# Kernel optimization log

Measured on AMD Instinct MI355X. Metric: run time of the kernel, lower is better.

## Reference

```python
import jax, jax.numpy as jnp
import numpy as np

B, T, D = 4, 8192, 1024
H = 16
HD = D // H  # 64
TOP_K = 64


def setup_inputs() -> dict:
    key = jax.random.key(0)
    ks = jax.random.split(key, 6)
    x = jax.random.normal(ks[0], (B, T, D), dtype=jnp.float32)
    # torch nn.Linear weights are [out, in]; y = x @ W.T
    Wq = jax.random.normal(ks[1], (D, D), dtype=jnp.float32) * 0.02
    Wk = jax.random.normal(ks[2], (D, D), dtype=jnp.float32) * 0.02
    Wv = jax.random.normal(ks[3], (D, D), dtype=jnp.float32) * 0.02
    Wo = jax.random.normal(ks[4], (D, D), dtype=jnp.float32) * 0.02
    # indexer: nn.Linear(head_dim, 1, bias=False) -> weight [1, HD]; keep as [HD]
    w_score = jax.random.normal(ks[5], (HD,), dtype=jnp.float32) * 0.02
    return {"x": x, "Wq": Wq, "Wk": Wk, "Wv": Wv, "Wo": Wo, "w_score": w_score}


def reference(x, Wq, Wk, Wv, Wo, w_score):
    b, t, d = x.shape
    top_k = min(TOP_K, t)
    # projections: [B,T,D] -> [B,H,T,HD]
    def proj(W):
        return jnp.einsum('btd,ed->bte', x, W).reshape(b, t, H, HD).transpose(0, 2, 1, 3)
    q = proj(Wq)
    k = proj(Wk)
    v = proj(Wv)
    # lightning indexer scores: [B,H,T]
    idx_scores = jnp.einsum('bhtd,d->bht', k, w_score)
    _, top_idx = jax.lax.top_k(idx_scores, top_k)  # [B,H,K]
    idx = top_idx[..., None]  # [B,H,K,1]
    k_sparse = jnp.take_along_axis(k, idx, axis=2)  # [B,H,K,HD]
    v_sparse = jnp.take_along_axis(v, idx, axis=2)
    scale = HD ** -0.5
    scores = jnp.einsum('bhtd,bhkd->bhtk', q, k_sparse) * scale  # [B,H,T,K]
    attn = jax.nn.softmax(scores, axis=-1)
    out = jnp.einsum('bhtk,bhkd->bhtd', attn, v_sparse)  # [B,H,T,HD]
    out = out.transpose(0, 2, 1, 3).reshape(b, t, d)
    return jnp.einsum('btd,ed->bte', out, Wo)
```

## Files before the change

kernel.cpp:

```cpp
#include <hip/hip_runtime.h>
#include <hip/hip_bf16.h>
#include <stdint.h>

#define NB 4
#define NT 8192
#define ND 1024
#define NH 16
#define NHD 64
#define NK 64
#define NM (NB*NT)

typedef __attribute__((ext_vector_type(4))) float f32x4;
typedef __attribute__((ext_vector_type(8))) short s16x8;
typedef const void __attribute__((address_space(1)))* gas1_t;
typedef void __attribute__((address_space(3)))* las3_t;

__device__ __forceinline__ float bf2f(ushort u) {
  union { uint32_t i; float f; } v; v.i = ((uint32_t)u) << 16; return v.f;
}
__device__ __forceinline__ ushort f2bf(float f) {
  union { float f; uint32_t i; } v; v.f = f;
  uint32_t r = v.i + 0x7FFFu + ((v.i >> 16) & 1u);
  return (ushort)(r >> 16);
}
__device__ __forceinline__ uint32_t f2ord(uint32_t u) {
  return (u & 0x80000000u) ? ~u : (u | 0x80000000u);
}

__global__ __launch_bounds__(256) void convert_w_kernel(
    const float* __restrict__ Wq, const float* __restrict__ Wk,
    const float* __restrict__ Wv, const float* __restrict__ Wo,
    ushort* __restrict__ wqb, ushort* __restrict__ wkb,
    ushort* __restrict__ wvb, ushort* __restrict__ wob) {
  int i = blockIdx.x * 256 + threadIdx.x;
  wqb[i] = f2bf(Wq[i]); wkb[i] = f2bf(Wk[i]);
  wvb[i] = f2bf(Wv[i]); wob[i] = f2bf(Wo[i]);
}

__global__ __launch_bounds__(256) void prep_u_kernel(
    const float* __restrict__ Wk, const float* __restrict__ wscore,
    ushort* __restrict__ uhi, ushort* __restrict__ ulo) {
  int e = (blockIdx.x & 3) * 256 + threadIdx.x;
  int h = blockIdx.x >> 2;
  float acc = 0.f;
  #pragma unroll 8
  for (int d = 0; d < NHD; ++d) acc += wscore[d] * Wk[(size_t)(h*NHD + d)*ND + e];
  ushort hv = f2bf(acc);
  uhi[h*ND + e] = hv;
  ulo[h*ND + e] = f2bf(acc - bf2f(hv));
}

__global__ __launch_bounds__(256) void prep_x_kernel(
    const float* __restrict__ x, const ushort* __restrict__ uhi,
    const ushort* __restrict__ ulo, ushort* __restrict__ xb,
    float* __restrict__ scores) {
  __shared__ float red[4][2][16][17];
  int t = threadIdx.x, w = t >> 6, l = t & 63;
  int tok0 = blockIdx.x * 32;
  int rs = l & 15, ks8 = (l >> 4) * 8;
  f32x4 acc[2];
  acc[0] = (f32x4){0.f,0.f,0.f,0.f};
  acc[1] = (f32x4){0.f,0.f,0.f,0.f};
  #pragma unroll 2
  for (int ks = 0; ks < 8; ++ks) {
    int kb = w * 256 + ks * 32;
    s16x8 bh = *(const s16x8*)(uhi + rs * ND + kb + ks8);
    s16x8 bl = *(const s16x8*)(ulo + rs * ND + kb + ks8);
    #pragma unroll
    for (int mi = 0; mi < 2; ++mi) {
      const float* xr = x + (size_t)(tok0 + mi*16 + rs) * ND + kb + ks8;
      f32x4 x0 = *(const f32x4*)xr;
      f32x4 x1 = *(const f32x4*)(xr + 4);
      s16x8 hi, lo;
      #pragma unroll
      for (int j = 0; j < 4; ++j) {
        ushort h0 = f2bf(x0[j]);
        hi[j] = (short)h0; lo[j] = (short)f2bf(x0[j] - bf2f(h0));
        ushort h1 = f2bf(x1[j]);
        hi[4+j] = (short)h1; lo[4+j] = (short)f2bf(x1[j] - bf2f(h1));
      }
      *(s16x8*)(xb + (size_t)(tok0 + mi*16 + rs) * ND + kb + ks8) = hi;
      acc[mi] = __builtin_amdgcn_mfma_f32_16x16x32_bf16(hi, bh, acc[mi], 0, 0, 0);
      acc[mi] = __builtin_amdgcn_mfma_f32_16x16x32_bf16(lo, bh, acc[mi], 0, 0, 0);
      acc[mi] = __builtin_amdgcn_mfma_f32_16x16x32_bf16(hi, bl, acc[mi], 0, 0, 0);
    }
  }
  #pragma unroll
  for (int mi = 0; mi < 2; ++mi)
    #pragma unroll
    for (int r = 0; r < 4; ++r)
      red[w][mi][(l >> 4) * 4 + r][l & 15] = acc[mi][r];
  __syncthreads();
  int boff = ((tok0 >> 13) << 4);
  int tt0 = tok0 & (NT - 1);
  #pragma unroll
  for (int it = 0; it < 2; ++it) {
    int tok = t & 31, h = (t >> 5) + it * 8;
    int mi = tok >> 4, row = tok & 15;
    float s = red[0][mi][row][h] + red[1][mi][row][h]
            + red[2][mi][row][h] + red[3][mi][row][h];
    scores[(size_t)(boff + h) * NT + tt0 + tok] = s;
  }
}

__global__ __launch_bounds__(256) void topk_kernel(
    const float* __restrict__ scores, int* __restrict__ tidx) {
  int bh = blockIdx.x, t = threadIdx.x;
  __shared__ uint32_t keys[NT];
  __shared__ int hist[4096];
  __shared__ uint32_t ck[512];
  __shared__ int ci[512];
  __shared__ int chunksum[256];
  __shared__ int s_binB, s_c0;
  __shared__ int cnt_hi, cnt_cand;

  for (int i = t; i < 4096; i += 256) hist[i] = 0;
  if (t == 0) { cnt_hi = 0; cnt_cand = 0; }
  __syncthreads();
  const uint4* sg = (const uint4*)(scores + (size_t)bh * NT);
  for (int i = t; i < NT/4; i += 256) {
    uint4 v = sg[i];
    uint32_t k0 = f2ord(v.x), k1 = f2ord(v.y), k2 = f2ord(v.z), k3 = f2ord(v.w);
    keys[i*4+0] = k0; keys[i*4+1] = k1; keys[i*4+2] = k2; keys[i*4+3] = k3;
    atomicAdd(&hist[k0 >> 20], 1); atomicAdd(&hist[k1 >> 20], 1);
    atomicAdd(&hist[k2 >> 20], 1); atomicAdd(&hist[k3 >> 20], 1);
  }
  __syncthreads();
  {
    int hi = 4095 - t * 16;
    int s = 0;
    #pragma unroll
    for (int j = 0; j < 16; ++j) s += hist[hi - j];
    chunksum[t] = s;
  }
  __syncthreads();
  if (t == 0) {
    int cum = 0, c = 0;
    while (cum + chunksum[c] < NK) { cum += chunksum[c]; ++c; }
    int bin = 4095 - c * 16;
    while (cum + hist[bin] < NK) { cum += hist[bin]; --bin; }
    s_binB = bin; s_c0 = cum;
  }
  __syncthreads();
  int binB = s_binB, c0 = s_c0;
  for (int i = t; i < NT; i += 256) {
    int b = keys[i] >> 20;
    if (b > binB) {
      int p = atomicAdd(&cnt_hi, 1);
      tidx[bh*NK + p] = i;
    } else if (b == binB) {
      int p = atomicAdd(&cnt_cand, 1);
      if (p < 512) { ck[p] = keys[i]; ci[p] = i; }
    }
  }
  __syncthreads();
  int nc = cnt_cand; if (nc > 512) nc = 512;
  int need = NK - c0;
  for (int p = t; p < nc; p += 256) {
    uint32_t myk = ck[p]; int myi = ci[p];
    int rank = 0;
    for (int j = 0; j < nc; ++j) {
      uint32_t kj = ck[j];
      rank += (kj > myk || (kj == myk && ci[j] < myi)) ? 1 : 0;
    }
    if (rank < need) tidx[bh*NK + c0 + rank] = myi;
  }
}

__global__ __launch_bounds__(256, 4) void sparse_kv_kernel(
    const ushort* __restrict__ xb, const ushort* __restrict__ wkb,
    const ushort* __restrict__ wvb, const int* __restrict__ tidx,
    ushort* __restrict__ ksp, ushort* __restrict__ vtsp) {
  int bh = blockIdx.x, gy = blockIdx.y;
  int b = bh >> 4, h = bh & 15;
  int t = threadIdx.x;
  __shared__ __align__(16) ushort xl[16][128];
  __shared__ int kid[16];
  if (t < 16) kid[t] = tidx[bh*NK + gy*16 + t];
  int d = t & 63, kq = t >> 6;
  float ak[4] = {0.f,0.f,0.f,0.f}, av[4] = {0.f,0.f,0.f,0.f};
  const ushort* wkr = wkb + (size_t)(h*NHD + d) * ND;
  const ushort* wvr = wvb + (size_t)(h*NHD + d) * ND;
  for (int kc = 0; kc < ND; kc += 128) {
    __syncthreads();
    {
      int row = t >> 4, c8 = (t & 15) * 8;
      *(uint4*)&xl[row][c8] = *(const uint4*)(xb + (size_t)(b*NT + kid[row]) * ND + kc + c8);
    }
    __syncthreads();
    #pragma unroll 1
    for (int sub = 0; sub < 8; ++sub) {
      s16x8 k0 = *(const s16x8*)(wkr + kc + sub*16);
      s16x8 k1 = *(const s16x8*)(wkr + kc + sub*16 + 8);
      s16x8 v0 = *(const s16x8*)(wvr + kc + sub*16);
      s16x8 v1 = *(const s16x8*)(wvr + kc + sub*16 + 8);
      float kf[16], vf2[16];
      #pragma unroll
      for (int j = 0; j < 8; ++j) {
        kf[j]  = bf2f((ushort)k0[j]); kf[8+j]  = bf2f((ushort)k1[j]);
        vf2[j] = bf2f((ushort)v0[j]); vf2[8+j] = bf2f((ushort)v1[j]);
      }
      #pragma unroll
      for (int kk = 0; kk < 4; ++kk) {
        #pragma unroll
        for (int j = 0; j < 16; ++j) {
          float xvv = bf2f(xl[kq*4 + kk][sub*16 + j]);
          ak[kk] += xvv * kf[j];
          av[kk] += xvv * vf2[j];
        }
      }
    }
  }
  #pragma unroll
  for (int kk = 0; kk < 4; ++kk) {
    int key = gy*16 + kq*4 + kk;
    ksp[((size_t)bh*NK + key)*NHD + d] = f2bf(ak[kk]);
    vtsp[((size_t)bh*NHD + d)*NK + key] = f2bf(av[kk]);
  }
}

template<int STORE_BF16>
__global__ __launch_bounds__(512, 2) void gemm8_kernel(
    const ushort* __restrict__ A, const ushort* __restrict__ Bw,
    void* __restrict__ Cout) {
  __shared__ __align__(16) char lds[131072];
  const int t = threadIdx.x, wid = t >> 6, l = t & 63;
  const int wr = wid >> 2, wc = wid & 3;
  int bid = blockIdx.x;
  int wg = (bid & 7) * 64 + (bid >> 3);
  int tm = wg >> 2, tn = wg & 3;
  const int K = 1024, N = 1024;
  const ushort* Ab = A + (size_t)tm * 256 * K;
  const ushort* Bb = Bw + (size_t)tn * 256 * K;
  const int skh  = ((l & 3) * 8) ^ (((l >> 5) & 1) << 4);
  const int srow = l >> 2;
  const int lane_off = (l & 15) * 64 + ((((l >> 4) * 8) ^ (((l >> 3) & 1) << 4)) * 2);
  f32x4 acc[8][4];
  #pragma unroll
  for (int i = 0; i < 8; ++i)
    #pragma unroll
    for (int j = 0; j < 4; ++j) acc[i][j] = (f32x4){0.f, 0.f, 0.f, 0.f};
  s16x8 afr[4][2], bfr[2][2];

#define STG(gbase, matoff, half, ktile, buf) do { \
    const ushort* _s = (gbase) + (size_t)((half)*128 + wid*16 + srow) * K + (ktile)*64 + skh; \
    int _d = (buf)*65536 + (matoff) + ((half)*128 + wid*16)*64; \
    __builtin_amdgcn_global_load_lds((gas1_t)_s, (las3_t)(lds + _d), 16, 0, 0); \
    __builtin_amdgcn_global_load_lds((gas1_t)(_s + 32), (las3_t)(lds + _d + 16384), 16, 0, 0); \
  } while (0)

#define RD_A(mh, kh, buf) do { \
    _Pragma("unroll") \
    for (int mi = 0; mi < 4; ++mi) \
      afr[mi][kh] = *(const s16x8*)(lds + (buf)*65536 + (kh)*16384 + \
                      ((((mh)*2 + wr)*64 + mi*16))*64 + lane_off); \
  } while (0)

#define RD_B(nh, kh, buf) do { \
    _Pragma("unroll") \
    for (int ni = 0; ni < 2; ++ni) \
      bfr[ni][kh] = *(const s16x8*)(lds + (buf)*65536 + 32768 + (kh)*16384 + \
                      (((nh)*128 + wc*32 + ni*16))*64 + lane_off); \
  } while (0)

#define MMAQH(mh, nh, kh) do { \
    __builtin_amdgcn_s_setprio(1); \
    _Pragma("unroll") \
    for (int mi = 0; mi < 4; ++mi) \
      _Pragma("unroll") \
      for (int ni = 0; ni < 2; ++ni) \
        acc[(mh)*4+mi][(nh)*2+ni] = __builtin_amdgcn_mfma_f32_16x16x32_bf16( \
            afr[mi][kh], bfr[ni][kh], acc[(mh)*4+mi][(nh)*2+ni], 0, 0, 0); \
    __builtin_amdgcn_s_setprio(0); \
  } while (0)

#define LG0() do { asm volatile("s_waitcnt lgkmcnt(0)" ::: "memory"); \
                   __builtin_amdgcn_sched_barrier(0); } while (0)
#define ENDPH() do { __builtin_amdgcn_sched_barrier(0); \
                     __builtin_amdgcn_s_barrier(); } while (0)

#define TILE(kt, bc, bn) do { \
  LG0(); MMAQH(0,0,0); RD_A(0,1,bc); RD_B(0,1,bc); ENDPH(); \
  LG0(); MMAQH(0,0,1); RD_B(1,0,bc); \
  if ((kt)+1 < 16) STG(Bb,32768,0,(kt)+1,bn); ENDPH(); \
  LG0(); MMAQH(0,1,0); RD_B(1,1,bc); ENDPH(); \
  LG0(); MMAQH(0,1,1); RD_A(1,0,bc); \
  if ((kt)+2 < 16) STG(Ab,0,0,(kt)+2,bc); ENDPH(); \
  LG0(); MMAQH(1,1,0); RD_A(1,1,bc); ENDPH(); \
  LG0(); MMAQH(1,1,1); RD_B(0,0,bc); \
  if ((kt)+2 < 16) STG(Bb,32768,1,(kt)+2,bc); ENDPH(); \
  LG0(); MMAQH(1,0,0); RD_B(0,1,bc); ENDPH(); \
  LG0(); MMAQH(1,0,1); \
  if ((kt) < 14)       { asm volatile("s_waitcnt vmcnt(4)" ::: "memory"); } \
  else if ((kt) == 14) { asm volatile("s_waitcnt vmcnt(0)" ::: "memory"); } \
  __builtin_amdgcn_sched_barrier(0); \
  __builtin_amdgcn_s_barrier(); \
  if ((kt)+1 < 16) { RD_A(0,0,bn); RD_B(0,0,bn); } \
  if ((kt)+2 < 16) STG(Ab,0,1,(kt)+2,bc); \
} while (0)

  STG(Ab,0,0,0,0); STG(Bb,32768,0,0,0); STG(Ab,0,1,0,0); STG(Bb,32768,1,0,0);
  STG(Ab,0,0,1,1); STG(Bb,32768,1,1,1); STG(Ab,0,1,1,1);
  asm volatile("s_waitcnt vmcnt(6)" ::: "memory");
  __builtin_amdgcn_s_barrier();
  RD_A(0,0,0); RD_B(0,0,0);

  for (int k2 = 0; k2 < 8; ++k2) {
    TILE(2*k2,     0, 1);
    TILE(2*k2 + 1, 1, 0);
  }
#undef TILE
#undef STG
#undef RD_A
#undef RD_B
#undef MMAQH
#undef LG0
#undef ENDPH

  #pragma unroll
  for (int mi8 = 0; mi8 < 8; ++mi8) {
    int grow = tm*256 + (((mi8 >> 2)*2 + wr)*64) + (mi8 & 3)*16 + (l >> 4)*4;
    #pragma unroll
    for (int ni4 = 0; ni4 < 4; ++ni4) {
      int gcol = tn*256 + (ni4 >> 1)*128 + wc*32 + (ni4 & 1)*16 + (l & 15);
      #pragma unroll
      for (int r = 0; r < 4; ++r) {
        size_t off = (size_t)(grow + r) * N + gcol;
        if (STORE_BF16) ((ushort*)Cout)[off] = f2bf(acc[mi8][ni4][r]);
        else            ((float*)Cout)[off]  = acc[mi8][ni4][r];
      }
    }
  }
}

__global__ __launch_bounds__(256, 2) void attn_kernel(
    const ushort* __restrict__ qg, const ushort* __restrict__ ksp,
    const ushort* __restrict__ vtsp, ushort* __restrict__ aout) {
  int bh = blockIdx.y;
  int b = bh >> 4, h = bh & 15;
  int t = threadIdx.x, w = t >> 6, l = t & 63;
  __shared__ __align__(16) ushort Pl[4][1024];
  const ushort* kb = ksp + (size_t)bh * NK * NHD;
  const ushort* vb = vtsp + (size_t)bh * NHD * NK;
  s16x8 kf[2][4], vf[2][4];
  #pragma unroll
  for (int ks = 0; ks < 2; ++ks)
    #pragma unroll
    for (int ni = 0; ni < 4; ++ni) {
      kf[ks][ni] = *(const s16x8*)&kb[(size_t)(ni*16 + (l & 15))*NHD + ks*32 + (l >> 4)*8];
      vf[ks][ni] = *(const s16x8*)&vb[(size_t)(ni*16 + (l & 15))*NK + ks*32 + (l >> 4)*8];
    }
  int rowbase = blockIdx.x * 256 + w * 64;
  #pragma unroll 1
  for (int mi = 0; mi < 4; ++mi) {
    int r0 = rowbase + mi * 16;
    s16x8 af[2];
    #pragma unroll
    for (int ks = 0; ks < 2; ++ks)
      af[ks] = *(const s16x8*)&qg[(size_t)(b*NT + r0 + (l & 15))*ND + h*NHD + ks*32 + (l >> 4)*8];
    f32x4 sc[4];
    #pragma unroll
    for (int ni = 0; ni < 4; ++ni) {
      f32x4 z; z[0]=0.f; z[1]=0.f; z[2]=0.f; z[3]=0.f;
      z = __builtin_amdgcn_mfma_f32_16x16x32_bf16(af[0], kf[0][ni], z, 0, 0, 0);
      sc[ni] = __builtin_amdgcn_mfma_f32_16x16x32_bf16(af[1], kf[1][ni], z, 0, 0, 0);
    }
    #pragma unroll
    for (int r = 0; r < 4; ++r) {
      float v0 = sc[0][r]*0.125f, v1 = sc[1][r]*0.125f;
      float v2 = sc[2][r]*0.125f, v3 = sc[3][r]*0.125f;
      float m = fmaxf(fmaxf(v0, v1), fmaxf(v2, v3));
      #pragma unroll
      for (int mm = 8; mm >= 1; mm >>= 1) m = fmaxf(m, __shfl_xor(m, mm, 64));
      float e0 = __expf(v0 - m), e1 = __expf(v1 - m);
      float e2 = __expf(v2 - m), e3 = __expf(v3 - m);
      float s = e0 + e1 + e2 + e3;
      #pragma unroll
      for (int mm = 8; mm >= 1; mm >>= 1) s += __shfl_xor(s, mm, 64);
      float inv = 1.f / s;
      int prow = (l >> 4)*4 + r;
      int lo = l & 7, hb = (l >> 3) & 1, sw = prow & 7;
      Pl[w][prow*64 + ((0 + hb) ^ sw)*8 + lo] = f2bf(e0 * inv);
      Pl[w][prow*64 + ((2 + hb) ^ sw)*8 + lo] = f2bf(e1 * inv);
      Pl[w][prow*64 + ((4 + hb) ^ sw)*8 + lo] = f2bf(e2 * inv);
      Pl[w][prow*64 + ((6 + hb) ^ sw)*8 + lo] = f2bf(e3 * inv);
    }
    s16x8 pf[2];
    #pragma unroll
    for (int ks = 0; ks < 2; ++ks)
      pf[ks] = *(const s16x8*)&Pl[w][(l & 15)*64 + ((ks*4 + (l >> 4)) ^ (l & 7))*8];
    f32x4 oc[4];
    #pragma unroll
    for (int ni = 0; ni < 4; ++ni) {
      f32x4 z; z[0]=0.f; z[1]=0.f; z[2]=0.f; z[3]=0.f;
      z = __builtin_amdgcn_mfma_f32_16x16x32_bf16(pf[0], vf[0][ni], z, 0, 0, 0);
      oc[ni] = __builtin_amdgcn_mfma_f32_16x16x32_bf16(pf[1], vf[1][ni], z, 0, 0, 0);
    }
    #pragma unroll
    for (int ni = 0; ni < 4; ++ni)
      #pragma unroll
      for (int r = 0; r < 4; ++r) {
        int row = r0 + (l >> 4)*4 + r;
        aout[(size_t)(b*NT + row)*ND + h*NHD + ni*16 + (l & 15)] = f2bf(oc[ni][r]);
      }
  }
}

extern "C" void kernel_launch(void* const* d_in, const int* in_sizes, int n_in,
                              void* d_out, int out_size, void* d_ws, size_t ws_size,
                              hipStream_t stream) {
  (void)in_sizes; (void)n_in; (void)out_size; (void)ws_size;
  const float* x  = (const float*)d_in[0];
  const float* Wq = (const float*)d_in[1];
  const float* Wk = (const float*)d_in[2];
  const float* Wv = (const float*)d_in[3];
  const float* Wo = (const float*)d_in[4];
  const float* wscore = (const float*)d_in[5];

  char* base = (char*)d_ws;
  ushort* xb     = (ushort*)(base + 0);
  ushort* qb     = (ushort*)(base + 67108864);
  float*  scores = (float*) (base + 134217728);
  ushort* uhi    = (ushort*)(base + 136314880);
  ushort* ulo    = (ushort*)(base + 136347648);
  ushort* wqb    = (ushort*)(base + 136380416);
  ushort* wkb    = (ushort*)(base + 138477568);
  ushort* wvb    = (ushort*)(base + 140574720);
  ushort* wob    = (ushort*)(base + 142671872);
  int*    tidx   = (int*)   (base + 144769024);
  ushort* ksp    = (ushort*)(base + 144785408);
  ushort* vtsp   = (ushort*)(base + 145309696);
  ushort* aout   = xb;

  convert_w_kernel<<<dim3(4096), dim3(256), 0, stream>>>(Wq, Wk, Wv, Wo, wqb, wkb, wvb, wob);
  prep_u_kernel<<<dim3(64), dim3(256), 0, stream>>>(Wk, wscore, uhi, ulo);
  prep_x_kernel<<<dim3(1024), dim3(256), 0, stream>>>(x, uhi, ulo, xb, scores);
  topk_kernel<<<dim3(64), dim3(256), 0, stream>>>(scores, tidx);
  sparse_kv_kernel<<<dim3(64, 4), dim3(256), 0, stream>>>(xb, wkb, wvb, tidx, ksp, vtsp);
  gemm8_kernel<1><<<dim3(512), dim3(512), 0, stream>>>(xb, wqb, (void*)qb);
  attn_kernel<<<dim3(32, 64), dim3(256), 0, stream>>>(qb, ksp, vtsp, aout);
  gemm8_kernel<0><<<dim3(512), dim3(512), 0, stream>>>(aout, wob, d_out);
}
```

Before: 295.7 us.

## Stage x tiles into LDS with async global_load_lds double buffering in prep_x

The prep_x kernel now streams 32x128 fp32 tiles of x into LDS via global_load_lds with a two-stage double buffer and an XOR swizzle, instead of each lane loading fp32 values straight from global memory. The k-loop is restructured over 128-wide chunks with explicit vmcnt waits and barriers. The bf16 copy of x is written with a separate coalesced per-thread pattern read from LDS. The intent is to overlap the global load of x with the MFMA scoring work and to coalesce both the reads and the bf16 writes. In exchange it adds LDS traffic and two block barriers per chunk.

```diff
diff --git a/kernel.cpp b/kernel.cpp
--- a/kernel.cpp
+++ b/kernel.cpp
@@ -54,37 +54,84 @@
     const float* __restrict__ x, const ushort* __restrict__ uhi,
     const ushort* __restrict__ ulo, ushort* __restrict__ xb,
     float* __restrict__ scores) {
+  __shared__ __align__(16) float Xs[2][32 * 128];
   __shared__ float red[4][2][16][17];
   int t = threadIdx.x, w = t >> 6, l = t & 63;
   int tok0 = blockIdx.x * 32;
-  int rs = l & 15, ks8 = (l >> 4) * 8;
+  int srow_[4]; int scol_[4];
+  #pragma unroll
+  for (int i = 0; i < 4; ++i) {
+    int row = (w * 4 + i) * 2 + (l >> 5);
+    int g = l & 31;
+    srow_[i] = row;
+    scol_[i] = (g ^ ((row & 7) << 1)) * 4;
+  }
+#define STGX(kc, buf) do { \
+    _Pragma("unroll") \
+    for (int i = 0; i < 4; ++i) \
+      __builtin_amdgcn_global_load_lds( \
+        (gas1_t)(x + (size_t)(tok0 + srow_[i]) * ND + (kc) * 128 + scol_[i]), \
+        (las3_t)((char*)&Xs[buf][0] + (w * 4 + i) * 1024 + (l & 63) * 0), \
+        16, 0, 0); \
+  } while (0)
+  int rs = l & 15, kq = l >> 4;
   f32x4 acc[2];
   acc[0] = (f32x4){0.f,0.f,0.f,0.f};
   acc[1] = (f32x4){0.f,0.f,0.f,0.f};
-  #pragma unroll 2
-  for (int ks = 0; ks < 8; ++ks) {
-    int kb = w * 256 + ks * 32;
-    s16x8 bh = *(const s16x8*)(uhi + rs * ND + kb + ks8);
-    s16x8 bl = *(const s16x8*)(ulo + rs * ND + kb + ks8);
+  STGX(0, 0);
+  STGX(1, 1);
+  for (int kc = 0; kc < 8; ++kc) {
+    if (kc < 7) { asm volatile("s_waitcnt vmcnt(4)" ::: "memory"); }
+    else        { asm volatile("s_waitcnt vmcnt(0)" ::: "memory"); }
+    __builtin_amdgcn_sched_barrier(0);
+    __builtin_amdgcn_s_barrier();
+    __builtin_amdgcn_sched_barrier(0);
+    const float* Xb = &Xs[kc & 1][0];
+    int kb = kc * 128;
+    s16x8 bh = *(const s16x8*)(uhi + rs * ND + kb + w * 32 + kq * 8);
+    s16x8 bl = *(const s16x8*)(ulo + rs * ND + kb + w * 32 + kq * 8);
     #pragma unroll
     for (int mi = 0; mi < 2; ++mi) {
-      const float* xr = x + (size_t)(tok0 + mi*16 + rs) * ND + kb + ks8;
-      f32x4 x0 = *(const f32x4*)xr;
-      f32x4 x1 = *(const f32x4*)(xr + 4);
+      int row = mi * 16 + rs;
+      int g0 = w * 8 + kq * 2;
+      int a0 = row * 128 + ((g0 ^ ((row & 7) << 1)) * 4);
+      f32x4 xv0 = *(const f32x4*)(Xb + a0);
+      f32x4 xv1 = *(const f32x4*)(Xb + a0 + 4);
       s16x8 hi, lo;
       #pragma unroll
       for (int j = 0; j < 4; ++j) {
-        ushort h0 = f2bf(x0[j]);
-        hi[j] = (short)h0; lo[j] = (short)f2bf(x0[j] - bf2f(h0));
-        ushort h1 = f2bf(x1[j]);
-        hi[4+j] = (short)h1; lo[4+j] = (short)f2bf(x1[j] - bf2f(h1));
-      }
-      *(s16x8*)(xb + (size_t)(tok0 + mi*16 + rs) * ND + kb + ks8) = hi;
+        ushort h0 = f2bf(xv0[j]);
+        hi[j] = (short)h0; lo[j] = (short)f2bf(xv0[j] - bf2f(h0));
+        ushort h1 = f2bf(xv1[j]);
+        hi[4+j] = (short)h1; lo[4+j] = (short)f2bf(xv1[j] - bf2f(h1));
+      }
       acc[mi] = __builtin_amdgcn_mfma_f32_16x16x32_bf16(hi, bh, acc[mi], 0, 0, 0);
       acc[mi] = __builtin_amdgcn_mfma_f32_16x16x32_bf16(lo, bh, acc[mi], 0, 0, 0);
       acc[mi] = __builtin_amdgcn_mfma_f32_16x16x32_bf16(hi, bl, acc[mi], 0, 0, 0);
     }
-  }
+    {
+      int rx = t >> 3, s = (rx & 7) << 1, g4 = (t & 7) * 4;
+      f32x4 v[4];
+      #pragma unroll
+      for (int j = 0; j < 4; ++j)
+        v[j] = *(const f32x4*)(Xb + rx * 128 + ((g4 + j) ^ s) * 4);
+      s16x8 o0, o1;
+      #pragma unroll
+      for (int j = 0; j < 4; ++j) {
+        o0[j]   = (short)f2bf(v[0][j]); o0[4+j] = (short)f2bf(v[1][j]);
+        o1[j]   = (short)f2bf(v[2][j]); o1[4+j] = (short)f2bf(v[3][j]);
+      }
+      ushort* xo = xb + (size_t)(tok0 + rx) * ND + kb + (t & 7) * 16;
+      *(s16x8*)xo = o0;
+      *(s16x8*)(xo + 8) = o1;
+    }
+    asm volatile("s_waitcnt lgkmcnt(0)" ::: "memory");
+    __builtin_amdgcn_sched_barrier(0);
+    __builtin_amdgcn_s_barrier();
+    __builtin_amdgcn_sched_barrier(0);
+    if (kc + 2 < 8) STGX(kc + 2, kc & 1);
+  }
+#undef STGX
   #pragma unroll
   for (int mi = 0; mi < 2; ++mi)
     #pragma unroll
```

New measurement: 294.5 us. Within noise of the previous version (-0.4%).
